# Optimization experiments

Hardware: AMD Instinct MI355X
Metric: run time of the kernel (lower is better)

The kernel has to match this reference:

```python
import jax, jax.numpy as jnp
import numpy as np

D_MODEL = 1024
MAX_NUM_LAYERS = 4


def setup_inputs() -> dict:
    key = jax.random.key(0)
    ks = jax.random.split(key, 8)
    S, B, D, L = 1024, 2, D_MODEL, 3
    w = lambda k: (jax.random.normal(k, (D, D), dtype=jnp.float32) * 0.02)
    return {
        "x": jax.random.normal(ks[0], (S, B, D), dtype=jnp.float32),
        "layer_outputs": jax.random.normal(ks[1], (L, S, B, D), dtype=jnp.float32),
        "Wq": w(ks[2]), "bq": jnp.zeros((D,), jnp.float32),
        "Wk": w(ks[3]), "bk": jnp.zeros((D,), jnp.float32),
        "Wv": w(ks[4]), "bv": jnp.zeros((D,), jnp.float32),
        "Wo": w(ks[5]), "bo": jnp.zeros((D,), jnp.float32),
        "layer_weights": jnp.ones((MAX_NUM_LAYERS + 1,), jnp.float32),
        "num_heads": 16,
    }


def reference(x, layer_outputs, Wq, bq, Wk, bk, Wv, bv, Wo, bo, layer_weights, num_heads):
    # x: [S, B, D]; layer_outputs: [L, S, B, D] (stacked prev layer outputs)
    S, B, D = x.shape
    H = num_heads
    hd = D // H
    scale = hd ** -0.5
    # q from x only: [S, B*H, hd] -> [BH, S, hd]
    q = (x @ Wq.T + bq).reshape(S, B * H, hd).transpose(1, 0, 2)
    # k/v from x and all previous layer outputs (shared K/V projections)
    xs = jnp.concatenate([x[None], layer_outputs], axis=0)          # [Lp1, S, B, D]
    Lp1 = xs.shape[0]
    k = (xs @ Wk.T + bk).reshape(Lp1, S, B * H, hd).transpose(0, 2, 1, 3)  # [Lp1, BH, S, hd]
    v = (xs @ Wv.T + bv).reshape(Lp1, S, B * H, hd).transpose(0, 2, 1, 3)
    # per-layer scores, softmax over the key axis (torch dim=-2 of stacked scores)
    scores = jnp.einsum('bqd,lbkd->lbqk', q, k) * scale             # [Lp1, BH, S, S]
    attn = jax.nn.softmax(scores, axis=-1)
    lw = jax.nn.softmax(layer_weights[:Lp1])                        # [Lp1]
    combined = jnp.einsum('l,lbqk,lbkd->bqd', lw, attn, v)          # [BH, S, hd]
    combined = combined.transpose(1, 0, 2).reshape(S, B, D)
    return combined @ Wo.T + bo
```

## Files before the change

### kernel.cpp

```cpp
#include <hip/hip_runtime.h>
#include <hip/hip_bf16.h>
#include <math.h>

#define S_LEN   1024
#define BATCH   2
#define DMODEL  1024
#define NHEADS  16
#define HDIM    64
#define BHEADS  32
#define LP1     4
#define ROWS_PL 2048

typedef __attribute__((ext_vector_type(8)))  short bf16x8;
typedef __attribute__((ext_vector_type(4)))  float f32x4;
typedef __attribute__((ext_vector_type(16))) float f32x16;

__device__ inline ushort bf16_rne(float a) {
    unsigned u = __float_as_uint(a);
    return (ushort)((u + 0x7FFFu + ((u >> 16) & 1u)) >> 16);
}
__device__ inline float bf16_up(ushort h) { return __uint_as_float(((unsigned)h) << 16); }
__device__ inline void split_bf16(float a, ushort &hi, ushort &lo) {
    hi = bf16_rne(a);
    lo = bf16_rne(a - bf16_up(hi));
}
__device__ inline uint pk_bf16(float a, float b) {
    float2 f; f.x = a; f.y = b;
    __hip_bfloat162 h = __float22bfloat162_rn(f);
    return *reinterpret_cast<uint*>(&h);
}
#if __has_builtin(__builtin_amdgcn_exp2f)
__device__ inline float fast_exp2(float x) { return __builtin_amdgcn_exp2f(x); }
#else
__device__ inline float fast_exp2(float x) { return exp2f(x); }
#endif

__device__ inline void permswap(uint &a, uint &b) {
    asm("v_permlane32_swap_b32 %0, %1" : "+v"(a), "+v"(b));
}

__device__ inline void glds16(const ushort* g, ushort* l) {
    __builtin_amdgcn_global_load_lds(
        (const __attribute__((address_space(1))) void*)g,
        (__attribute__((address_space(3))) void*)l, 16, 0, 0);
}

#define SCLF 0.18033688011112042f

__global__ __launch_bounds__(256)
void presplit(const float* __restrict__ x, const float* __restrict__ lo,
              const float* __restrict__ Wq, const float* __restrict__ Wk,
              const float* __restrict__ Wv, const float* __restrict__ Wo,
              ushort* __restrict__ XsH, ushort* __restrict__ WH,
              ushort* __restrict__ WL)
{
    const int z = blockIdx.z;
    const float* src; ushort* dh; ushort* dl = nullptr; int n;
    if (z == 0)      { src = x;  dh = XsH;           n = 2097152; }
    else if (z == 1) { src = lo; dh = XsH + 2097152; n = 6291456; }
    else {
        const float* wsrc[4] = { Wq, Wk, Wv, Wo };
        src = wsrc[z - 2];
        dh = WH + (size_t)(z - 2) * 1048576;
        if (z == 2 || z == 5) dl = WL + (size_t)(z - 2) * 1048576;
        n = 1048576;
    }
    const int i = (blockIdx.x * 256 + threadIdx.x) * 8;
    if (i >= n) return;
    float v[8];
    *(float4*)&v[0] = *(const float4*)(src + i);
    *(float4*)&v[4] = *(const float4*)(src + i + 4);
    ushort h[8];
    #pragma unroll
    for (int j = 0; j < 8; ++j) h[j] = bf16_rne(v[j]);
    *(uint4*)(dh + i) = *(uint4*)h;
    if (dl) {
        ushort l[8];
        #pragma unroll
        for (int j = 0; j < 8; ++j) l[j] = bf16_rne(v[j] - bf16_up(h[j]));
        *(uint4*)(dl + i) = *(uint4*)l;
    }
}

template<int MODE>
__global__ __launch_bounds__(256)
void proj_g(const ushort* __restrict__ Abf,
            const ushort* __restrict__ Bhg, const ushort* __restrict__ Blg,
            const float* __restrict__ bias,
            float* __restrict__ outf, ushort* __restrict__ outh,
            ushort* __restrict__ outl)
{
    __shared__ ushort smem[3 * 2048];
    ushort* Ah = smem;
    ushort* Bh = smem + 2048;
    ushort* Bl = smem + 4096;

    const int fid = blockIdx.x;
    const int nt = (fid & 7) * 2 + ((fid >> 3) & 1);
    const int mt = fid >> 4;
    const int m0 = mt * 64, n0 = nt * 64;

    const int t  = threadIdx.x;
    const int wv = t >> 6, lane = t & 63;
    const int quad = lane >> 4, r = lane & 15;
    const int wm = wv & 1, wn = wv >> 1;
    const int mBase = wm * 32, nBase = wn * 32;

    const int lrow = lane >> 2;
    const int lch  = ((lane & 3) ^ (lrow & 3)) * 8;
    const ushort* Asrc  = Abf + (size_t)(m0 + wv * 16 + lrow) * DMODEL + lch;
    const ushort* Bhsrc = Bhg + (size_t)(n0 + wv * 16 + lrow) * DMODEL + lch;
    const ushort* Blsrc = Blg + (size_t)(n0 + wv * 16 + lrow) * DMODEL + lch;
    ushort* lA  = Ah + wv * 512;
    ushort* lBh = Bh + wv * 512;
    ushort* lBl = Bl + wv * 512;

    const int q0x = (quad ^ (r & 3)) << 3;
    f32x4 acc[2][2];
    #pragma unroll
    for (int i = 0; i < 2; ++i)
        #pragma unroll
        for (int j = 0; j < 2; ++j) acc[i][j] = (f32x4){0.f, 0.f, 0.f, 0.f};

    for (int k0 = 0; k0 < DMODEL; k0 += 32) {
        glds16(Asrc + k0, lA);
        glds16(Bhsrc + k0, lBh);
        glds16(Blsrc + k0, lBl);
        __syncthreads();
        bf16x8 fa[2], fbh[2], fbl[2];
        #pragma unroll
        for (int i = 0; i < 2; ++i)
            fa[i] = *(const bf16x8*)&Ah[(mBase + i * 16 + r) * 32 + q0x];
        #pragma unroll
        for (int j = 0; j < 2; ++j) {
            fbh[j] = *(const bf16x8*)&Bh[(nBase + j * 16 + r) * 32 + q0x];
            fbl[j] = *(const bf16x8*)&Bl[(nBase + j * 16 + r) * 32 + q0x];
        }
        #pragma unroll
        for (int i = 0; i < 2; ++i)
            #pragma unroll
            for (int j = 0; j < 2; ++j) {
                acc[i][j] = __builtin_amdgcn_mfma_f32_16x16x32_bf16(fa[i], fbh[j], acc[i][j], 0, 0, 0);
                acc[i][j] = __builtin_amdgcn_mfma_f32_16x16x32_bf16(fa[i], fbl[j], acc[i][j], 0, 0, 0);
            }
        __syncthreads();
    }

    const int cn = lane & 15;
    #pragma unroll
    for (int j = 0; j < 2; ++j) {
        const int n = n0 + nBase + j * 16 + cn;
        const float bv = bias[n];
        #pragma unroll
        for (int i = 0; i < 2; ++i) {
            const int mrow = m0 + mBase + i * 16 + quad * 4;
            #pragma unroll
            for (int g = 0; g < 4; ++g) {
                const int m = mrow + g;
                if (MODE == 1) {
                    outf[(size_t)m * DMODEL + n] = acc[i][j][g] + bv;
                } else {
                    const float val = (acc[i][j][g] + bv) * SCLF;
                    const int s = m >> 1, b = m & 1;
                    const int bh = b * 16 + (n >> 6), e = n & 63;
                    const size_t idx = (((size_t)bh * S_LEN) + s) * HDIM + e;
                    ushort hi, lov; split_bf16(val, hi, lov);
                    outh[idx] = hi; outl[idx] = lov;
                }
            }
        }
    }
}

__global__ __launch_bounds__(256, 4)
void proj_kv(const ushort* __restrict__ XsH,
             const ushort* __restrict__ KWh, const ushort* __restrict__ VWh,
             const float* __restrict__ bk, const float* __restrict__ bv,
             ushort* __restrict__ kout, ushort* __restrict__ vout)
{
    __shared__ ushort smem[10240];
    ushort* Ah = smem;
    ushort* Bp = smem + 2048;

    const int t  = threadIdx.x;
    const int m0 = blockIdx.y * 64, n0 = blockIdx.x * 128;
    const int lyr = m0 >> 11;

    const int wv = t >> 6, lane = t & 63;
    const int quad = lane >> 4, r = lane & 15;
    const int wm = wv & 1, wn = wv >> 1;
    const int mBase = wm * 32, nBase = wn * 64;

    const int lrow = lane >> 2;
    const int lch  = ((lane & 3) ^ (lrow & 3)) * 8;

    const ushort* Asrc = XsH + (size_t)(m0 + wv * 16 + lrow) * DMODEL + lch;
    const ushort* Bw[2] = { KWh, VWh };
    const ushort* Bsrc[2][2];
    #pragma unroll
    for (int p = 0; p < 2; ++p)
        #pragma unroll
        for (int seg = 0; seg < 2; ++seg)
            Bsrc[p][seg] = Bw[p] + (size_t)(n0 + wv * 32 + seg * 16 + lrow) * DMODEL + lch;

    const int q0x = (quad ^ (r & 3)) << 3;

    f32x4 aK[2][4], aV[2][4];
    #pragma unroll
    for (int i = 0; i < 2; ++i)
        #pragma unroll
        for (int j = 0; j < 4; ++j) {
            aK[i][j] = (f32x4){0.f, 0.f, 0.f, 0.f};
            aV[i][j] = (f32x4){0.f, 0.f, 0.f, 0.f};
        }

    for (int k0 = 0; k0 < DMODEL; k0 += 32) {
        glds16(Asrc + k0, Ah + wv * 512);
        #pragma unroll
        for (int p = 0; p < 2; ++p)
            #pragma unroll
            for (int seg = 0; seg < 2; ++seg)
                glds16(Bsrc[p][seg] + k0, Bp + p * 4096 + (wv * 2 + seg) * 512);
        __syncthreads();

        bf16x8 fa[2];
        #pragma unroll
        for (int i = 0; i < 2; ++i)
            fa[i] = *(const bf16x8*)&Ah[(mBase + i * 16 + r) * 32 + q0x];
        #pragma unroll
        for (int j = 0; j < 4; ++j) {
            const int off = (nBase + j * 16 + r) * 32 + q0x;
            const bf16x8 fkh = *(const bf16x8*)&Bp[off];
            const bf16x8 fvh = *(const bf16x8*)&Bp[4096 + off];
            #pragma unroll
            for (int i = 0; i < 2; ++i) {
                aK[i][j] = __builtin_amdgcn_mfma_f32_16x16x32_bf16(fa[i], fkh, aK[i][j], 0, 0, 0);
                aV[i][j] = __builtin_amdgcn_mfma_f32_16x16x32_bf16(fa[i], fvh, aV[i][j], 0, 0, 0);
            }
        }
        __syncthreads();
    }

    const int cn = lane & 15;

    #pragma unroll
    for (int j = 0; j < 4; ++j) {
        const int n = n0 + nBase + j * 16 + cn;
        const float bb = bk[n];
        #pragma unroll
        for (int i = 0; i < 2; ++i) {
            #pragma unroll
            for (int g = 0; g < 4; ++g) {
                const int m = m0 + mBase + i * 16 + quad * 4 + g;
                const int rem = m & 2047, s = rem >> 1, b = rem & 1;
                const int bh = lyr * 32 + b * 16 + (n >> 6);
                kout[(((size_t)bh * S_LEN) + s) * HDIM + (n & 63)] = bf16_rne(aK[i][j][g] + bb);
            }
        }
    }

    ushort* T = smem;
    __syncthreads();
    #pragma unroll
    for (int j = 0; j < 4; ++j) {
        const int nloc = nBase + j * 16 + cn;
        const float bb = bv[n0 + nloc];
        #pragma unroll
        for (int i = 0; i < 2; ++i) {
            #pragma unroll
            for (int g = 0; g < 4; ++g) {
                const int mloc = mBase + i * 16 + quad * 4 + g;
                T[nloc * 66 + mloc] = bf16_rne(aV[i][j][g] + bb);
            }
        }
    }
    __syncthreads();
    {
        const int nloc = t >> 1, bsel = t & 1;
        const int n = n0 + nloc, h = n >> 6, e = n & 63;
        const int s0g = (m0 & 2047) >> 1;
        const int bhI = lyr * 32 + bsel * 16 + h;
        ushort* dst = vout + ((size_t)bhI * HDIM + e) * S_LEN + s0g;
        #pragma unroll
        for (int c = 0; c < 4; ++c) {
            ushort tmp[8];
            #pragma unroll
            for (int j = 0; j < 8; ++j)
                tmp[j] = T[nloc * 66 + 2 * (c * 8 + j) + bsel];
            *(uint4*)(dst + c * 8) = *(uint4*)tmp;
        }
    }
}

__global__ __launch_bounds__(256, 2)
void attn_mfma(const ushort* __restrict__ qhg, const ushort* __restrict__ qlg,
               const ushort* __restrict__ kh, const ushort* __restrict__ vth,
               const float* __restrict__ lwraw, float* __restrict__ part)
{
    const int t    = threadIdx.x;
    const int wv   = t >> 6, lane = t & 63;
    const int half = lane >> 5, lid = lane & 31;

    const int fid  = blockIdx.x;
    const int xcd  = fid & 7, slot = fid >> 3;
    const int pair = xcd * 16 + (slot >> 2);
    const int qt   = slot & 3;
    const int bh   = pair & 31, l = pair >> 5;
    const int qbase = qt * 256 + wv * 64;

    float wl;
    {
        float v[LP1], wm = -3.0e38f;
        #pragma unroll
        for (int i = 0; i < LP1; ++i) { v[i] = lwraw[i]; wm = fmaxf(wm, v[i]); }
        float ws = 0.f;
        #pragma unroll
        for (int i = 0; i < LP1; ++i) { v[i] = __expf(v[i] - wm); ws += v[i]; }
        wl = v[l] / ws;
    }

    bf16x8 qh[2][4], ql[2][4];
    #pragma unroll
    for (int u = 0; u < 2; ++u) {
        const size_t qoff = ((size_t)bh * S_LEN + qbase + u * 32 + lid) * HDIM + half * 8;
        #pragma unroll
        for (int es = 0; es < 4; ++es) {
            qh[u][es] = *(const bf16x8*)(qhg + qoff + es * 16);
            ql[u][es] = *(const bf16x8*)(qlg + qoff + es * 16);
        }
    }

    f32x16 o[2][2];
    #pragma unroll
    for (int u = 0; u < 2; ++u)
        #pragma unroll
        for (int dg = 0; dg < 2; ++dg)
            #pragma unroll
            for (int i = 0; i < 16; ++i) o[u][dg][i] = 0.f;
    float ls[2] = {0.f, 0.f};

    const size_t kvo = (size_t)(l * BHEADS + bh) * S_LEN * HDIM;
    const ushort* kbase = kh + kvo + (size_t)lid * HDIM + half * 8;
    const ushort* vbase = vth + kvo + (size_t)lid * S_LEN + half * 8;

    bf16x8 kb[4], kn[4];
    #pragma unroll
    for (int es = 0; es < 4; ++es)
        kb[es] = *(const bf16x8*)(kbase + es * 16);
    #pragma unroll
    for (int es = 0; es < 4; ++es)
        kn[es] = *(const bf16x8*)(kbase + (size_t)32 * HDIM + es * 16);

    f32x16 sa[2];
    #pragma unroll
    for (int u = 0; u < 2; ++u)
        #pragma unroll
        for (int i = 0; i < 16; ++i) sa[u][i] = 0.f;
    #pragma unroll
    for (int es = 0; es < 4; ++es)
        #pragma unroll
        for (int u = 0; u < 2; ++u) {
            sa[u] = __builtin_amdgcn_mfma_f32_32x32x16_bf16(kb[es], qh[u][es], sa[u], 0, 0, 0);
            sa[u] = __builtin_amdgcn_mfma_f32_32x32x16_bf16(kb[es], ql[u][es], sa[u], 0, 0, 0);
        }

    for (int kt = 0; kt < 32; ++kt) {
        bf16x8 vb[2][2];
        {
            const ushort* vp = vbase + kt * 32;
            #pragma unroll
            for (int ks = 0; ks < 2; ++ks)
                #pragma unroll
                for (int dg = 0; dg < 2; ++dg)
                    vb[ks][dg] = *(const bf16x8*)(vp + (size_t)dg * (32 * S_LEN) + ks * 16);
        }

        bf16x8 pf[2][2];
        #pragma unroll
        for (int ks = 0; ks < 2; ++ks) {
            #pragma unroll
            for (int u = 0; u < 2; ++u) {
                const float p0 = fast_exp2(sa[u][8 * ks + 0]);
                const float p1 = fast_exp2(sa[u][8 * ks + 1]);
                const float p2 = fast_exp2(sa[u][8 * ks + 2]);
                const float p3 = fast_exp2(sa[u][8 * ks + 3]);
                const float p4 = fast_exp2(sa[u][8 * ks + 4]);
                const float p5 = fast_exp2(sa[u][8 * ks + 5]);
                const float p6 = fast_exp2(sa[u][8 * ks + 6]);
                const float p7 = fast_exp2(sa[u][8 * ks + 7]);
                ls[u] += ((p0 + p1) + (p2 + p3)) + ((p4 + p5) + (p6 + p7));

                uint a0 = pk_bf16(p0, p1);
                uint a1 = pk_bf16(p2, p3);
                uint b0 = pk_bf16(p4, p5);
                uint b1 = pk_bf16(p6, p7);
                permswap(a0, b0);
                permswap(a1, b1);
                union { uint w[4]; bf16x8 v; } pu;
                pu.w[0] = a0; pu.w[1] = a1; pu.w[2] = b0; pu.w[3] = b1;
                pf[ks][u] = pu.v;
            }
        }

        #pragma unroll
        for (int es = 0; es < 4; ++es) kb[es] = kn[es];
        {
            const ushort* kp = kbase + (size_t)((kt + 2) & 31) * 32 * HDIM;
            #pragma unroll
            for (int es = 0; es < 4; ++es) kn[es] = *(const bf16x8*)(kp + es * 16);
        }

        #pragma unroll
        for (int u = 0; u < 2; ++u)
            #pragma unroll
            for (int i = 0; i < 16; ++i) sa[u][i] = 0.f;
        __builtin_amdgcn_s_setprio(1);
        #pragma unroll
        for (int es = 0; es < 4; ++es)
            #pragma unroll
            for (int u = 0; u < 2; ++u) {
                sa[u] = __builtin_amdgcn_mfma_f32_32x32x16_bf16(kb[es], qh[u][es], sa[u], 0, 0, 0);
                sa[u] = __builtin_amdgcn_mfma_f32_32x32x16_bf16(kb[es], ql[u][es], sa[u], 0, 0, 0);
            }
        __builtin_amdgcn_s_setprio(0);

        __builtin_amdgcn_s_setprio(1);
        #pragma unroll
        for (int ks = 0; ks < 2; ++ks)
            #pragma unroll
            for (int dg = 0; dg < 2; ++dg)
                #pragma unroll
                for (int u = 0; u < 2; ++u)
                    o[u][dg] = __builtin_amdgcn_mfma_f32_32x32x16_bf16(vb[ks][dg], pf[ks][u], o[u][dg], 0, 0, 0);
        __builtin_amdgcn_s_setprio(0);
    }

    const int b = bh >> 4, hh = bh & 15;
    #pragma unroll
    for (int u = 0; u < 2; ++u) {
        float lsv = ls[u];
        lsv += __shfl_xor(lsv, 32);
        const float sc = wl / lsv;
        const int q = qbase + u * 32 + lid;
        float* pb = part + (size_t)l * (ROWS_PL * DMODEL)
                  + ((size_t)q * BATCH + b) * DMODEL + hh * HDIM;
        #pragma unroll
        for (int dg = 0; dg < 2; ++dg)
            #pragma unroll
            for (int rq = 0; rq < 4; ++rq) {
                float4 vv;
                vv.x = o[u][dg][rq * 4 + 0] * sc;
                vv.y = o[u][dg][rq * 4 + 1] * sc;
                vv.z = o[u][dg][rq * 4 + 2] * sc;
                vv.w = o[u][dg][rq * 4 + 3] * sc;
                *(float4*)(pb + dg * 32 + rq * 8 + half * 4) = vv;
            }
    }
}

__global__ __launch_bounds__(256)
void sum_y(const float* __restrict__ part, ushort* __restrict__ YH)
{
    const int i = (blockIdx.x * 256 + threadIdx.x) * 8;
    float acc[8];
    #pragma unroll
    for (int c = 0; c < 2; ++c) {
        float4 s = *(const float4*)(part + i + c * 4);
        #pragma unroll
        for (int l = 1; l < LP1; ++l) {
            const float4 p = *(const float4*)(part + (size_t)l * 2097152 + i + c * 4);
            s.x += p.x; s.y += p.y; s.z += p.z; s.w += p.w;
        }
        acc[c * 4 + 0] = s.x; acc[c * 4 + 1] = s.y;
        acc[c * 4 + 2] = s.z; acc[c * 4 + 3] = s.w;
    }
    uint out[4];
    #pragma unroll
    for (int c = 0; c < 4; ++c) out[c] = pk_bf16(acc[c * 2], acc[c * 2 + 1]);
    *(uint4*)(YH + i) = *(uint4*)out;
}

extern "C" void kernel_launch(void* const* d_in, const int* in_sizes, int n_in,
                              void* d_out, int out_size, void* d_ws, size_t ws_size,
                              hipStream_t stream) {
    const float* x  = (const float*)d_in[0];
    const float* lo = (const float*)d_in[1];
    const float* Wq = (const float*)d_in[2];
    const float* bq = (const float*)d_in[3];
    const float* Wk = (const float*)d_in[4];
    const float* bk = (const float*)d_in[5];
    const float* Wv = (const float*)d_in[6];
    const float* bv = (const float*)d_in[7];
    const float* Wo = (const float*)d_in[8];
    const float* bo = (const float*)d_in[9];
    const float* lw = (const float*)d_in[10];
    float* out = (float*)d_out;

    char* ws = (char*)d_ws;
    ushort* XsH  = (ushort*)(ws);
    ushort* WH   = (ushort*)(ws + 16777216);
    ushort* WL   = (ushort*)(ws + 25165824);
    ushort* qhb  = (ushort*)(ws + 33554432);
    ushort* qlb  = (ushort*)(ws + 37748736);
    ushort* khb  = (ushort*)(ws + 41943040);
    ushort* vthb = (ushort*)(ws + 58720256);
    float*  part = (float*)(ws + 75497472);
    ushort* YH   = (ushort*)(ws + 109051904);

    dim3 blk(256);
    presplit<<<dim3(3072, 1, 6), blk, 0, stream>>>(x, lo, Wq, Wk, Wv, Wo, XsH, WH, WL);
    proj_g<0><<<dim3(512), blk, 0, stream>>>(XsH, WH, WL, bq, nullptr, qhb, qlb);
    proj_kv<<<dim3(8, 128), blk, 0, stream>>>(XsH,
        WH + 1048576, WH + 2097152, bk, bv, khb, vthb);
    attn_mfma<<<dim3(512), blk, 0, stream>>>(qhb, qlb, khb, vthb, lw, part);
    sum_y<<<dim3(1024), blk, 0, stream>>>(part, YH);
    proj_g<1><<<dim3(512), blk, 0, stream>>>(YH, WH + 3145728, WL + 3145728, bo, out, nullptr, nullptr);
}
```

Baseline: 284.4 us.

## Store K and V in MFMA-fragment-major layout for coalesced attention loads

```diff
diff --git a/kernel.cpp b/kernel.cpp
--- a/kernel.cpp
+++ b/kernel.cpp
@@ -247,14 +247,20 @@
     for (int j = 0; j < 4; ++j) {
         const int n = n0 + nBase + j * 16 + cn;
         const float bb = bk[n];
+        const int e    = n & 63;
+        const int es_k = e >> 4, half_k = (e >> 3) & 1, j_k = e & 7;
+        const int h    = n >> 6;
         #pragma unroll
         for (int i = 0; i < 2; ++i) {
             #pragma unroll
             for (int g = 0; g < 4; ++g) {
                 const int m = m0 + mBase + i * 16 + quad * 4 + g;
                 const int rem = m & 2047, s = rem >> 1, b = rem & 1;
-                const int bh = lyr * 32 + b * 16 + (n >> 6);
-                kout[(((size_t)bh * S_LEN) + s) * HDIM + (n & 63)] = bf16_rne(aK[i][j][g] + bb);
+                const int bhI = lyr * 32 + b * 16 + h;
+                const int kt  = s >> 5;
+                const int lnk = half_k * 32 + (s & 31);
+                kout[(size_t)bhI * 65536 + (size_t)(kt * 4 + es_k) * 512 + lnk * 8 + j_k]
+                    = bf16_rne(aK[i][j][g] + bb);
             }
         }
     }
@@ -277,17 +283,21 @@
     __syncthreads();
     {
         const int nloc = t >> 1, bsel = t & 1;
-        const int n = n0 + nloc, h = n >> 6, e = n & 63;
+        const int n = n0 + nloc, h = n >> 6;
+        const int e = n & 63;
+        const int dg = e >> 5, lid_v = e & 31;
         const int s0g = (m0 & 2047) >> 1;
+        const int kt  = s0g >> 5;
         const int bhI = lyr * 32 + bsel * 16 + h;
-        ushort* dst = vout + ((size_t)bhI * HDIM + e) * S_LEN + s0g;
+        ushort* dstb = vout + (size_t)bhI * 65536 + (size_t)kt * 2048;
         #pragma unroll
         for (int c = 0; c < 4; ++c) {
             ushort tmp[8];
             #pragma unroll
             for (int j = 0; j < 8; ++j)
                 tmp[j] = T[nloc * 66 + 2 * (c * 8 + j) + bsel];
-            *(uint4*)(dst + c * 8) = *(uint4*)tmp;
+            const int ks = c >> 1, hv = c & 1;
+            *(uint4*)(dstb + (ks * 2 + dg) * 512 + (hv * 32 + lid_v) * 8) = *(uint4*)tmp;
         }
     }
 }
@@ -340,16 +350,16 @@
     float ls[2] = {0.f, 0.f};
 
     const size_t kvo = (size_t)(l * BHEADS + bh) * S_LEN * HDIM;
-    const ushort* kbase = kh + kvo + (size_t)lid * HDIM + half * 8;
-    const ushort* vbase = vth + kvo + (size_t)lid * S_LEN + half * 8;
+    const ushort* kfb = kh  + kvo + (size_t)lane * 8;
+    const ushort* vfb = vth + kvo + (size_t)lane * 8;
 
     bf16x8 kb[4], kn[4];
     #pragma unroll
     for (int es = 0; es < 4; ++es)
-        kb[es] = *(const bf16x8*)(kbase + es * 16);
+        kb[es] = *(const bf16x8*)(kfb + es * 512);
     #pragma unroll
     for (int es = 0; es < 4; ++es)
-        kn[es] = *(const bf16x8*)(kbase + (size_t)32 * HDIM + es * 16);
+        kn[es] = *(const bf16x8*)(kfb + 2048 + es * 512);
 
     f32x16 sa[2];
     #pragma unroll
@@ -367,12 +377,12 @@
     for (int kt = 0; kt < 32; ++kt) {
         bf16x8 vb[2][2];
         {
-            const ushort* vp = vbase + kt * 32;
+            const ushort* vp = vfb + (size_t)kt * 2048;
             #pragma unroll
             for (int ks = 0; ks < 2; ++ks)
                 #pragma unroll
                 for (int dg = 0; dg < 2; ++dg)
-                    vb[ks][dg] = *(const bf16x8*)(vp + (size_t)dg * (32 * S_LEN) + ks * 16);
+                    vb[ks][dg] = *(const bf16x8*)(vp + (ks * 2 + dg) * 512);
         }
 
         bf16x8 pf[2][2];
@@ -405,9 +415,9 @@
         #pragma unroll
         for (int es = 0; es < 4; ++es) kb[es] = kn[es];
         {
-            const ushort* kp = kbase + (size_t)((kt + 2) & 31) * 32 * HDIM;
-            #pragma unroll
-            for (int es = 0; es < 4; ++es) kn[es] = *(const bf16x8*)(kp + es * 16);
+            const ushort* kp = kfb + (size_t)((kt + 2) & 31) * 2048;
+            #pragma unroll
+            for (int es = 0; es < 4; ++es) kn[es] = *(const bf16x8*)(kp + es * 512);
         }
 
         #pragma unroll
```

Result: faster. 259.0 us (-8.9%).
